# Performance work log

Measured on AMD Instinct MI355X. Metric: run time of the kernel, lower is better.

Reference implementation:

```python
import jax, jax.numpy as jnp
import numpy as np

D_MODEL = 1024
N_HEADS = 16
HEAD_DIM = D_MODEL // N_HEADS
WINDOW = 128
NEG = -1e9


def setup_inputs() -> dict:
    key = jax.random.key(0)
    ks = jax.random.split(key, 9)
    s = 1.0 / np.sqrt(D_MODEL)
    x = jax.random.normal(ks[0], (1, 4096, D_MODEL), dtype=jnp.float32)
    Wq = jax.random.uniform(ks[1], (D_MODEL, D_MODEL), jnp.float32, -s, s)
    bq = jax.random.uniform(ks[2], (D_MODEL,), jnp.float32, -s, s)
    Wk = jax.random.uniform(ks[3], (D_MODEL, D_MODEL), jnp.float32, -s, s)
    bk = jax.random.uniform(ks[4], (D_MODEL,), jnp.float32, -s, s)
    Wv = jax.random.uniform(ks[5], (D_MODEL, D_MODEL), jnp.float32, -s, s)
    bv = jax.random.uniform(ks[6], (D_MODEL,), jnp.float32, -s, s)
    Wo = jax.random.uniform(ks[7], (D_MODEL, D_MODEL), jnp.float32, -s, s)
    bo = jax.random.uniform(ks[8], (D_MODEL,), jnp.float32, -s, s)
    return {"x": x, "Wq": Wq, "bq": bq, "Wk": Wk, "bk": bk,
            "Wv": Wv, "bv": bv, "Wo": Wo, "bo": bo}


def reference(x, Wq, bq, Wk, bk, Wv, bv, Wo, bo):
    B, S, _ = x.shape
    scale = 1.0 / np.sqrt(HEAD_DIM)

    def heads(W, b):
        # [B,S,D] -> [B,H,S,hd]  (torch Linear: x @ W.T + b)
        return (x @ W.T + b).reshape(B, S, N_HEADS, HEAD_DIM).transpose(0, 2, 1, 3)

    q = heads(Wq, bq)
    k = heads(Wk, bk)
    v = heads(Wv, bv)

    scores = jnp.einsum('bhqd,bhkd->bhqk', q, k) * scale  # [B,H,S,S]
    i = jnp.arange(S)
    window_mask = jnp.abs(i[:, None] - i[None, :]) <= (WINDOW // 2)  # [S,S]
    scores = jnp.where(window_mask[None, None], scores, NEG)
    attn = jax.nn.softmax(scores, axis=-1)
    ctx = jnp.einsum('bhqk,bhkd->bhqd', attn, v)
    ctx = ctx.transpose(0, 2, 1, 3).reshape(B, S, D_MODEL)
    return ctx @ Wo.T + bo
```

## Files before the change

### kernel.cpp

```cpp
#include <hip/hip_runtime.h>

typedef __bf16 bf16;
typedef __bf16 bf16x8 __attribute__((ext_vector_type(8)));
typedef __bf16 bf16x4 __attribute__((ext_vector_type(4)));
typedef float floatx4 __attribute__((ext_vector_type(4)));

#define SEQ 4096
#define DM 1024
#define NH 16
#define HD 64
#define SD 3072

__device__ __forceinline__ floatx4 mfma32(bf16x8 a, bf16x8 b, floatx4 c) {
    return __builtin_amdgcn_mfma_f32_16x16x32_bf16(a, b, c, 0, 0, 0);
}

__device__ __forceinline__ bf16x8 load8(const bf16* p) {
    return *(const bf16x8*)p;
}

__device__ __forceinline__ void async_ld16(const bf16* g, bf16* l) {
    __builtin_amdgcn_global_load_lds(
        (const __attribute__((address_space(1))) unsigned int*)g,
        (__attribute__((address_space(3))) unsigned int*)l,
        16, 0, 0);
}

__global__ __launch_bounds__(256) void prep_kernel(
    const float* __restrict__ x,  const float* __restrict__ Wq,
    const float* __restrict__ Wk, const float* __restrict__ Wv,
    const float* __restrict__ Wo, const float* __restrict__ bq,
    const float* __restrict__ bk, const float* __restrict__ bv,
    bf16* __restrict__ xb, bf16* __restrict__ Wcat,
    bf16* __restrict__ Wob, float* __restrict__ bcat)
{
    const int WN8 = 131072;
    const int XN8 = 524288;
    int b = blockIdx.x;
    if (b == 4096) {
        for (int k = threadIdx.x; k < 3 * DM; k += 256)
            bcat[k] = k < DM ? bq[k] : (k < 2 * DM ? bk[k - DM] : bv[k - 2 * DM]);
        return;
    }
    int c = b * 256 + threadIdx.x;
    const float* src; bf16* dst;
    if (c < XN8)              { src = x;  dst = xb; }
    else if (c < XN8 + WN8)   { src = Wq; dst = Wcat;                 c -= XN8; }
    else if (c < XN8 + 2*WN8) { src = Wk; dst = Wcat + (size_t)DM*DM;     c -= XN8 + WN8; }
    else if (c < XN8 + 3*WN8) { src = Wv; dst = Wcat + (size_t)2*DM*DM;   c -= XN8 + 2*WN8; }
    else                      { src = Wo; dst = Wob;                  c -= XN8 + 3*WN8; }
    float4 a = ((const float4*)src)[2 * c], d2 = ((const float4*)src)[2 * c + 1];
    bf16x8 o;
    o[0] = (bf16)a.x;  o[1] = (bf16)a.y;  o[2] = (bf16)a.z;  o[3] = (bf16)a.w;
    o[4] = (bf16)d2.x; o[5] = (bf16)d2.y; o[6] = (bf16)d2.z; o[7] = (bf16)d2.w;
    *(bf16x8*)(dst + 8 * (size_t)c) = o;
}

template <int BM, typename TOUT>
__global__ __launch_bounds__(256) void gemm_lds_kernel(
    const bf16* __restrict__ A,
    const bf16* __restrict__ B,
    const float* __restrict__ bias,
    TOUT* __restrict__ C,
    int M, int N, int K)
{
    constexpr int MI = BM / 32;
    __shared__ bf16 As[BM * 32];
    __shared__ bf16 Bs[128 * 32];

    const int tid  = threadIdx.x;
    const int wave = tid >> 6;
    const int lane = tid & 63;
    const int l15  = lane & 15;
    const int quad = lane >> 4;
    const int m0 = blockIdx.x * BM;
    const int n0 = blockIdx.y * 128;

    const int wm = (wave & 1) * (BM / 2);
    const int wn = (wave >> 1) * 64;

    const int lrow = lane >> 2;
    const int lcol = (lane & 3) * 8;

    const bf16* aptr[2]; bf16* alds[2]; int na = 0;
#pragma unroll
    for (int c = wave; c < BM / 16; c += 4) {
        aptr[na] = A + (size_t)(m0 + c * 16 + lrow) * K + lcol;
        alds[na] = As + c * 512;
        ++na;
    }
    const bf16* bptr[2]; bf16* blds[2];
    {
        int i = 0;
#pragma unroll
        for (int c = wave; c < 8; c += 4) {
            bptr[i] = B + (size_t)(n0 + c * 16 + lrow) * K + lcol;
            blds[i] = Bs + c * 512;
            ++i;
        }
    }

    floatx4 acc[MI][4] = {};

    for (int k0 = 0; k0 < K; k0 += 32) {
        __syncthreads();
#pragma unroll
        for (int i = 0; i < 2; ++i)
            if (i < na) async_ld16(aptr[i] + k0, alds[i]);
#pragma unroll
        for (int i = 0; i < 2; ++i)
            async_ld16(bptr[i] + k0, blds[i]);
        __syncthreads();

        bf16x8 af[MI], bfr[4];
#pragma unroll
        for (int i = 0; i < MI; ++i)
            af[i] = load8(As + (wm + i * 16 + l15) * 32 + quad * 8);
#pragma unroll
        for (int j = 0; j < 4; ++j)
            bfr[j] = load8(Bs + (wn + j * 16 + l15) * 32 + quad * 8);
#pragma unroll
        for (int i = 0; i < MI; ++i)
#pragma unroll
            for (int j = 0; j < 4; ++j)
                acc[i][j] = mfma32(bfr[j], af[i], acc[i][j]);
    }

#pragma unroll
    for (int i = 0; i < MI; ++i) {
        int xm = m0 + wm + i * 16 + l15;
#pragma unroll
        for (int j = 0; j < 4; ++j) {
            int cn = n0 + wn + j * 16 + quad * 4;
            float4 bv = *(const float4*)(bias + cn);
            float v0 = acc[i][j][0] + bv.x;
            float v1 = acc[i][j][1] + bv.y;
            float v2 = acc[i][j][2] + bv.z;
            float v3 = acc[i][j][3] + bv.w;
            if constexpr (sizeof(TOUT) == 2) {
                bf16x4 o = {(bf16)v0, (bf16)v1, (bf16)v2, (bf16)v3};
                *(bf16x4*)((bf16*)C + (size_t)xm * N + cn) = o;
            } else {
                float4 o = {v0, v1, v2, v3};
                *(float4*)((float*)C + (size_t)xm * N + cn) = o;
            }
        }
    }
}

__global__ __launch_bounds__(256, 4) void swattn_kernel(
    const bf16* __restrict__ QKV,
    bf16* __restrict__ ctx)
{
    __shared__ bf16 Vt[64][216];
    __shared__ bf16 Pc[4][16][40];
    __shared__ float lred[4][16];

    const int tid  = threadIdx.x;
    const int wave = tid >> 6;
    const int lane = tid & 63;
    const int l15  = lane & 15;
    const int quad = lane >> 4;
    const int q0   = blockIdx.x * 64;
    const int h    = blockIdx.y;
    const int hoff = h * HD;
    const int kbase = q0 - 64;

    for (int task = tid; task < 432; task += 256) {
        int kg = task % 54, dc = task / 54;
        bf16x8 r[4];
#pragma unroll
        for (int i = 0; i < 4; ++i) {
            int gk = kbase + 4 * kg + i;
            gk = gk < 0 ? 0 : (gk > SEQ - 1 ? SEQ - 1 : gk);
            r[i] = load8(QKV + (size_t)gk * SD + 2048 + hoff + dc * 8);
        }
#pragma unroll
        for (int j = 0; j < 8; ++j) {
            bf16x4 w = { r[0][j], r[1][j], r[2][j], r[3][j] };
            *(bf16x4*)&Vt[dc * 8 + j][4 * kg] = w;
        }
    }

    const int qrow = q0 + wave * 16 + l15;
    const bf16* qb = QKV + (size_t)qrow * SD + hoff + quad * 8;
    bf16x8 aq0 = load8(qb), aq1 = load8(qb + 32);

    const int ws = kbase + wave * 16;
    floatx4 s[9];
#pragma unroll
    for (int st = 0; st < 9; ++st) {
        int kr = ws + st * 16 + l15;
        int kc2 = kr < 0 ? 0 : (kr > SEQ - 1 ? SEQ - 1 : kr);
        const bf16* kp = QKV + (size_t)kc2 * SD + 1024 + hoff + quad * 8;
        bf16x8 b0 = load8(kp), b1 = load8(kp + 32);
        floatx4 acc = {};
        acc = mfma32(aq0, b0, acc);
        acc = mfma32(aq1, b1, acc);
        s[st] = acc;
    }

#pragma unroll
    for (int r = 0; r < 4; ++r) {
        int row = quad * 4 + r;
        float mx = -INFINITY;
#pragma unroll
        for (int st = 0; st < 9; ++st) {
            int j = st * 16 + l15;
            int gk = ws + j;
            bool ok = (j >= row) && (j <= 128 + row) && (gk >= 0) && (gk < SEQ);
            float v = ok ? s[st][r] * 0.125f : -1e30f;
            s[st][r] = v;
            mx = fmaxf(mx, v);
        }
        mx = fmaxf(mx, __shfl_xor(mx, 1));
        mx = fmaxf(mx, __shfl_xor(mx, 2));
        mx = fmaxf(mx, __shfl_xor(mx, 4));
        mx = fmaxf(mx, __shfl_xor(mx, 8));
        float sum = 0.f;
#pragma unroll
        for (int st = 0; st < 9; ++st) {
            float p = __expf(s[st][r] - mx);
            s[st][r] = p;
            sum += p;
        }
        sum += __shfl_xor(sum, 1);
        sum += __shfl_xor(sum, 2);
        sum += __shfl_xor(sum, 4);
        sum += __shfl_xor(sum, 8);
        lred[wave][row] = sum;
    }

    __syncthreads();

    floatx4 ot[4] = {};
#pragma unroll
    for (int kc = 0; kc < 5; ++kc) {
#pragma unroll
        for (int r = 0; r < 4; ++r) {
            int row = quad * 4 + r;
            Pc[wave][row][l15] = (bf16)s[2 * kc][r];
            if (kc < 4)
                Pc[wave][row][16 + l15] = (bf16)s[2 * kc + 1][r];
            else
                Pc[wave][row][16 + l15] = (bf16)0.f;
        }
        bf16x8 pb = load8(&Pc[wave][l15][quad * 8]);
#pragma unroll
        for (int dt = 0; dt < 4; ++dt) {
            bf16x8 va = load8(&Vt[dt * 16 + l15][wave * 16 + kc * 32 + quad * 8]);
            ot[dt] = mfma32(va, pb, ot[dt]);
        }
    }

    float linv = 1.0f / lred[wave][l15];
#pragma unroll
    for (int dt = 0; dt < 4; ++dt) {
        bf16x4 o4;
#pragma unroll
        for (int r = 0; r < 4; ++r) o4[r] = (bf16)(ot[dt][r] * linv);
        *(bf16x4*)(ctx + (size_t)qrow * DM + hoff + dt * 16 + quad * 4) = o4;
    }
}

extern "C" void kernel_launch(void* const* d_in, const int* in_sizes, int n_in,
                              void* d_out, int out_size, void* d_ws, size_t ws_size,
                              hipStream_t stream) {
    const float* x  = (const float*)d_in[0];
    const float* Wq = (const float*)d_in[1];
    const float* bq = (const float*)d_in[2];
    const float* Wk = (const float*)d_in[3];
    const float* bk = (const float*)d_in[4];
    const float* Wv = (const float*)d_in[5];
    const float* bv = (const float*)d_in[6];
    const float* Wo = (const float*)d_in[7];
    const float* bo = (const float*)d_in[8];
    float* out = (float*)d_out;

    const size_t XN = (size_t)SEQ * DM;
    const size_t WN = (size_t)DM * DM;

    bf16* xb   = (bf16*)d_ws;
    bf16* Wcat = xb + XN;
    bf16* Wob  = Wcat + 3 * WN;
    bf16* QKV  = Wob + WN;
    bf16* ctx  = QKV + 3 * XN;
    float* bcat = (float*)(ctx + XN);

    prep_kernel<<<4097, 256, 0, stream>>>(x, Wq, Wk, Wv, Wo, bq, bk, bv,
                                          xb, Wcat, Wob, bcat);

    gemm_lds_kernel<128, bf16><<<dim3(SEQ / 128, SD / 128), 256, 0, stream>>>(
        xb, Wcat, bcat, QKV, SEQ, SD, DM);

    swattn_kernel<<<dim3(SEQ / 64, NH), 256, 0, stream>>>(QKV, ctx);

    gemm_lds_kernel<64, float><<<dim3(SEQ / 64, DM / 128), 256, 0, stream>>>(
        ctx, Wob, bo, out, SEQ, DM, DM);
}
```

Before: 186.0 us.

## Emit head-major Q/K and transposed V from QKV GEMM, swizzle LDS, deepen K-tile

The QKV projection GEMM now writes Q and K in head-major [head][seq][64] layout and V transposed as [dim][seq], with guard padding. The attention kernel can then read V directly from global memory instead of transposing it into shared memory, and it drops a block barrier. Both GEMMs move to a 64-wide K tile with an XOR-style swizzled LDS layout, aimed at fewer bank conflicts and fewer barriers. The trade-off is strided scalar-ish stores for V^T, unguarded V reads at the sequence edges that rely on the guard padding, and ctx aliasing the xb buffer.

```diff
diff --git a/kernel.cpp b/kernel.cpp
--- a/kernel.cpp
+++ b/kernel.cpp
@@ -1,4 +1,5 @@
 #include <hip/hip_runtime.h>
+#include <type_traits>
 
 typedef __bf16 bf16;
 typedef __bf16 bf16x8 __attribute__((ext_vector_type(8)));
@@ -9,7 +10,7 @@
 #define DM 1024
 #define NH 16
 #define HD 64
-#define SD 3072
+#define GUARD 64
 
 __device__ __forceinline__ floatx4 mfma32(bf16x8 a, bf16x8 b, floatx4 c) {
     return __builtin_amdgcn_mfma_f32_16x16x32_bf16(a, b, c, 0, 0, 0);
@@ -56,17 +57,117 @@
     *(bf16x8*)(dst + 8 * (size_t)c) = o;
 }
 
-template <int BM, typename TOUT>
-__global__ __launch_bounds__(256) void gemm_lds_kernel(
+__global__ __launch_bounds__(256) void gemm_qkv_kernel(
     const bf16* __restrict__ A,
     const bf16* __restrict__ B,
     const float* __restrict__ bias,
-    TOUT* __restrict__ C,
+    bf16* __restrict__ Qh, bf16* __restrict__ Kh, bf16* __restrict__ Vt)
+{
+    constexpr int K = DM;
+    __shared__ bf16 As[128 * 64];
+    __shared__ bf16 Bs[128 * 64];
+
+    const int tid  = threadIdx.x;
+    const int wave = tid >> 6;
+    const int lane = tid & 63;
+    const int l15  = lane & 15;
+    const int quad = lane >> 4;
+    const int m0 = blockIdx.x * 128;
+    const int n0 = blockIdx.y * 128;
+    const int wm = (wave & 1) * 64;
+    const int wn = (wave >> 1) * 64;
+
+    const int lr = lane >> 3;
+    const int gc = ((lane & 7) - lr) & 7;
+
+    const bf16* aptr[4]; bf16* alds[4];
+    const bf16* bptr[4]; bf16* blds[4];
+#pragma unroll
+    for (int i = 0; i < 4; ++i) {
+        int ci = wave + 4 * i;
+        aptr[i] = A + (size_t)(m0 + ci * 8 + lr) * K + gc * 8;
+        alds[i] = As + ci * 512;
+        bptr[i] = B + (size_t)(n0 + ci * 8 + lr) * K + gc * 8;
+        blds[i] = Bs + ci * 512;
+    }
+
+    floatx4 acc[4][4] = {};
+    const int sw0 = (quad + (l15 & 7)) & 7;
+    const bool qk = (n0 < 2 * DM);
+
+    auto kloop = [&](auto swtag) {
+        constexpr bool SW = decltype(swtag)::value;
+        for (int k0 = 0; k0 < K; k0 += 64) {
+            __syncthreads();
+#pragma unroll
+            for (int i = 0; i < 4; ++i) async_ld16(aptr[i] + k0, alds[i]);
+#pragma unroll
+            for (int i = 0; i < 4; ++i) async_ld16(bptr[i] + k0, blds[i]);
+            __syncthreads();
+#pragma unroll
+            for (int h = 0; h < 2; ++h) {
+                const int so = ((sw0 + 4 * h) & 7) * 8;
+                bf16x8 af[4], bfr[4];
+#pragma unroll
+                for (int i = 0; i < 4; ++i)
+                    af[i] = load8(As + (wm + i * 16 + l15) * 64 + so);
+#pragma unroll
+                for (int j = 0; j < 4; ++j)
+                    bfr[j] = load8(Bs + (wn + j * 16 + l15) * 64 + so);
+#pragma unroll
+                for (int i = 0; i < 4; ++i)
+#pragma unroll
+                    for (int j = 0; j < 4; ++j)
+                        acc[i][j] = SW ? mfma32(bfr[j], af[i], acc[i][j])
+                                       : mfma32(af[i], bfr[j], acc[i][j]);
+            }
+        }
+    };
+    if (qk) kloop(std::true_type{}); else kloop(std::false_type{});
+
+    const int nb = n0 + wn;
+    if (qk) {
+        bf16* dst = (nb < DM) ? Qh : Kh;
+        const int hh = ((nb < DM) ? nb : nb - DM) >> 6;
+#pragma unroll
+        for (int i = 0; i < 4; ++i) {
+            int s = m0 + wm + i * 16 + l15;
+            bf16* row = dst + ((size_t)hh * SEQ + s) * 64;
+#pragma unroll
+            for (int j = 0; j < 4; ++j) {
+                int d4 = j * 16 + quad * 4;
+                float4 bv = *(const float4*)(bias + nb + d4);
+                bf16x4 o = {(bf16)(acc[i][j][0] + bv.x), (bf16)(acc[i][j][1] + bv.y),
+                            (bf16)(acc[i][j][2] + bv.z), (bf16)(acc[i][j][3] + bv.w)};
+                *(bf16x4*)(row + d4) = o;
+            }
+        }
+    } else {
+#pragma unroll
+        for (int j = 0; j < 4; ++j) {
+            int vrow = (nb - 2 * DM) + j * 16 + l15;
+            float bvs = bias[nb + j * 16 + l15];
+            bf16* row = Vt + (size_t)vrow * SEQ;
+#pragma unroll
+            for (int i = 0; i < 4; ++i) {
+                int s4 = m0 + wm + i * 16 + quad * 4;
+                bf16x4 o = {(bf16)(acc[i][j][0] + bvs), (bf16)(acc[i][j][1] + bvs),
+                            (bf16)(acc[i][j][2] + bvs), (bf16)(acc[i][j][3] + bvs)};
+                *(bf16x4*)(row + s4) = o;
+            }
+        }
+    }
+}
+
+template <int BM, typename TOUT>
+__global__ __launch_bounds__(256) void gemm_sw_kernel(
+    const bf16* __restrict__ A, const bf16* __restrict__ B,
+    const float* __restrict__ bias, TOUT* __restrict__ C,
     int M, int N, int K)
 {
     constexpr int MI = BM / 32;
-    __shared__ bf16 As[BM * 32];
-    __shared__ bf16 Bs[128 * 32];
+    __shared__ bf16 As[BM * 64];
+    __shared__ bf16 Bs[128 * 64];
 
     const int tid  = threadIdx.x;
     const int wave = tid >> 6;
@@ -75,55 +176,53 @@
     const int quad = lane >> 4;
     const int m0 = blockIdx.x * BM;
     const int n0 = blockIdx.y * 128;
-
     const int wm = (wave & 1) * (BM / 2);
     const int wn = (wave >> 1) * 64;
 
-    const int lrow = lane >> 2;
-    const int lcol = (lane & 3) * 8;
-
-    const bf16* aptr[2]; bf16* alds[2]; int na = 0;
-#pragma unroll
-    for (int c = wave; c < BM / 16; c += 4) {
-        aptr[na] = A + (size_t)(m0 + c * 16 + lrow) * K + lcol;
-        alds[na] = As + c * 512;
-        ++na;
-    }
-    const bf16* bptr[2]; bf16* blds[2];
-    {
-        int i = 0;
-#pragma unroll
-        for (int c = wave; c < 8; c += 4) {
-            bptr[i] = B + (size_t)(n0 + c * 16 + lrow) * K + lcol;
-            blds[i] = Bs + c * 512;
-            ++i;
-        }
+    const int lr = lane >> 3;
+    const int gc = ((lane & 7) - lr) & 7;
+
+    const bf16* aptr[MI]; bf16* alds[MI];
+    const bf16* bptr[4];  bf16* blds[4];
+#pragma unroll
+    for (int i = 0; i < MI; ++i) {
+        int ci = wave + 4 * i;
+        aptr[i] = A + (size_t)(m0 + ci * 8 + lr) * K + gc * 8;
+        alds[i] = As + ci * 512;
+    }
+#pragma unroll
+    for (int j = 0; j < 4; ++j) {
+        int cj = wave + 4 * j;
+        bptr[j] = B + (size_t)(n0 + cj * 8 + lr) * K + gc * 8;
+        blds[j] = Bs + cj * 512;
     }
 
     floatx4 acc[MI][4] = {};
-
-    for (int k0 = 0; k0 < K; k0 += 32) {
+    const int sw0 = (quad + (l15 & 7)) & 7;
+
+    for (int k0 = 0; k0 < K; k0 += 64) {
         __syncthreads();
 #pragma unroll
-        for (int i = 0; i < 2; ++i)
-            if (i < na) async_ld16(aptr[i] + k0, alds[i]);
-#pragma unroll
-        for (int i = 0; i < 2; ++i)
-            async_ld16(bptr[i] + k0, blds[i]);
+        for (int i = 0; i < MI; ++i) async_ld16(aptr[i] + k0, alds[i]);
+#pragma unroll
+        for (int j = 0; j < 4; ++j) async_ld16(bptr[j] + k0, blds[j]);
         __syncthreads();
-
-        bf16x8 af[MI], bfr[4];
-#pragma unroll
-        for (int i = 0; i < MI; ++i)
-            af[i] = load8(As + (wm + i * 16 + l15) * 32 + quad * 8);
-#pragma unroll
-        for (int j = 0; j < 4; ++j)
-            bfr[j] = load8(Bs + (wn + j * 16 + l15) * 32 + quad * 8);
-#pragma unroll
-        for (int i = 0; i < MI; ++i)
+#pragma unroll
+        for (int h = 0; h < 2; ++h) {
+            const int so = ((sw0 + 4 * h) & 7) * 8;
+            bf16x8 af[MI], bfr[4];
+#pragma unroll
+            for (int i = 0; i < MI; ++i)
+                af[i] = load8(As + (wm + i * 16 + l15) * 64 + so);
 #pragma unroll
             for (int j = 0; j < 4; ++j)
-                acc[i][j] = mfma32(bfr[j], af[i], acc[i][j]);
+                bfr[j] = load8(Bs + (wn + j * 16 + l15) * 64 + so);
+#pragma unroll
+            for (int i = 0; i < MI; ++i)
+#pragma unroll
+                for (int j = 0; j < 4; ++j)
+                    acc[i][j] = mfma32(bfr[j], af[i], acc[i][j]);
+        }
     }
 
 #pragma unroll
@@ -148,11 +247,10 @@
     }
 }
 
-__global__ __launch_bounds__(256, 4) void swattn_kernel(
-    const bf16* __restrict__ QKV,
-    bf16* __restrict__ ctx)
+__global__ __launch_bounds__(256) void swattn_kernel(
+    const bf16* __restrict__ Qh, const bf16* __restrict__ Kh,
+    const bf16* __restrict__ Vt, bf16* __restrict__ ctx)
 {
-    __shared__ bf16 Vt[64][216];
     __shared__ bf16 Pc[4][16][40];
     __shared__ float lred[4][16];
 
@@ -164,35 +262,22 @@
     const int q0   = blockIdx.x * 64;
     const int h    = blockIdx.y;
     const int hoff = h * HD;
-    const int kbase = q0 - 64;
-
-    for (int task = tid; task < 432; task += 256) {
-        int kg = task % 54, dc = task / 54;
-        bf16x8 r[4];
-#pragma unroll
-        for (int i = 0; i < 4; ++i) {
-            int gk = kbase + 4 * kg + i;
-            gk = gk < 0 ? 0 : (gk > SEQ - 1 ? SEQ - 1 : gk);
-            r[i] = load8(QKV + (size_t)gk * SD + 2048 + hoff + dc * 8);
-        }
-#pragma unroll
-        for (int j = 0; j < 8; ++j) {
-            bf16x4 w = { r[0][j], r[1][j], r[2][j], r[3][j] };
-            *(bf16x4*)&Vt[dc * 8 + j][4 * kg] = w;
-        }
-    }
+
+    const bf16* qhead = Qh + (size_t)h * SEQ * 64;
+    const bf16* khead = Kh + (size_t)h * SEQ * 64;
+    const bf16* vhead = Vt + (size_t)hoff * SEQ;
 
     const int qrow = q0 + wave * 16 + l15;
-    const bf16* qb = QKV + (size_t)qrow * SD + hoff + quad * 8;
-    bf16x8 aq0 = load8(qb), aq1 = load8(qb + 32);
-
-    const int ws = kbase + wave * 16;
+    bf16x8 aq0 = load8(qhead + (size_t)qrow * 64 + quad * 8);
+    bf16x8 aq1 = load8(qhead + (size_t)qrow * 64 + quad * 8 + 32);
+
+    const int ws = q0 - 64 + wave * 16;
     floatx4 s[9];
 #pragma unroll
     for (int st = 0; st < 9; ++st) {
         int kr = ws + st * 16 + l15;
         int kc2 = kr < 0 ? 0 : (kr > SEQ - 1 ? SEQ - 1 : kr);
-        const bf16* kp = QKV + (size_t)kc2 * SD + 1024 + hoff + quad * 8;
+        const bf16* kp = khead + (size_t)kc2 * 64 + quad * 8;
         bf16x8 b0 = load8(kp), b1 = load8(kp + 32);
         floatx4 acc = {};
         acc = mfma32(aq0, b0, acc);
@@ -231,8 +316,6 @@
         lred[wave][row] = sum;
     }
 
-    __syncthreads();
-
     floatx4 ot[4] = {};
 #pragma unroll
     for (int kc = 0; kc < 5; ++kc) {
@@ -240,16 +323,14 @@
         for (int r = 0; r < 4; ++r) {
             int row = quad * 4 + r;
             Pc[wave][row][l15] = (bf16)s[2 * kc][r];
-            if (kc < 4)
-                Pc[wave][row][16 + l15] = (bf16)s[2 * kc + 1][r];
-            else
-                Pc[wave][row][16 + l15] = (bf16)0.f;
+            Pc[wave][row][16 + l15] = (kc < 4) ? (bf16)s[2 * kc + 1][r] : (bf16)0.f;
         }
         bf16x8 pb = load8(&Pc[wave][l15][quad * 8]);
 #pragma unroll
         for (int dt = 0; dt < 4; ++dt) {
-            bf16x8 va = load8(&Vt[dt * 16 + l15][wave * 16 + kc * 32 + quad * 8]);
-            ot[dt] = mfma32(va, pb, ot[dt]);
+            const bf16* vp = vhead + (ptrdiff_t)(dt * 16 + l15) * SEQ
+                                   + (ptrdiff_t)(ws + kc * 32 + quad * 8);
+            ot[dt] = mfma32(load8(vp), pb, ot[dt]);
         }
     }
 
@@ -280,21 +361,24 @@
     const size_t XN = (size_t)SEQ * DM;
     const size_t WN = (size_t)DM * DM;
 
-    bf16* xb   = (bf16*)d_ws;
-    bf16* Wcat = xb + XN;
-    bf16* Wob  = Wcat + 3 * WN;
-    bf16* QKV  = Wob + WN;
-    bf16* ctx  = QKV + 3 * XN;
-    float* bcat = (float*)(ctx + XN);
+    bf16* xb    = (bf16*)d_ws;
+    bf16* Wcat  = xb + XN;
+    bf16* Wob   = Wcat + 3 * WN;
+    bf16* Qh    = Wob + WN;
+    bf16* Kh    = Qh + XN;
+    bf16* VtRaw = Kh + XN;
+    bf16* Vtb   = VtRaw + GUARD;
+    float* bcat = (float*)(VtRaw + XN + 2 * GUARD + 128);
+    bf16* ctx   = xb;
 
     prep_kernel<<<4097, 256, 0, stream>>>(x, Wq, Wk, Wv, Wo, bq, bk, bv,
                                           xb, Wcat, Wob, bcat);
 
-    gemm_lds_kernel<128, bf16><<<dim3(SEQ / 128, SD / 128), 256, 0, stream>>>(
-        xb, Wcat, bcat, QKV, SEQ, SD, DM);
-
-    swattn_kernel<<<dim3(SEQ / 64, NH), 256, 0, stream>>>(QKV, ctx);
-
-    gemm_lds_kernel<64, float><<<dim3(SEQ / 64, DM / 128), 256, 0, stream>>>(
+    gemm_qkv_kernel<<<dim3(SEQ / 128, 24), 256, 0, stream>>>(
+        xb, Wcat, bcat, Qh, Kh, Vtb);
+
+    swattn_kernel<<<dim3(SEQ / 64, NH), 256, 0, stream>>>(Qh, Kh, Vtb, ctx);
+
+    gemm_sw_kernel<64, float><<<dim3(SEQ / 64, DM / 128), 256, 0, stream>>>(
         ctx, Wob, bo, out, SEQ, DM, DM);
 }
```

Result: faster. 171.0 us (-8.1%).
